# Performance work log

Hardware: AMD Instinct MI355X
Metric: run time of the kernel (lower is better)

Reference implementation:

```python
import jax, jax.numpy as jnp
import numpy as np

ALPHA_LO = float(np.exp(-1.0 / 5.0))   # 0.8187
ALPHA_HI = float(np.exp(-1.0 / 25.0))  # 0.9608
BN_EPS = 1e-5

B, T, D_IN, H = 32, 2000, 512, 512


def setup_inputs() -> dict:
    key = jax.random.key(0)
    ks = jax.random.split(key, 5)
    x = jax.random.normal(ks[0], (B, T, D_IN), dtype=jnp.float32)
    W = jax.random.normal(ks[1], (H, D_IN), dtype=jnp.float32) / np.sqrt(D_IN)
    b = jax.random.normal(ks[2], (H,), dtype=jnp.float32) * 0.01
    alpha = jax.random.uniform(ks[3], (H,), dtype=jnp.float32,
                               minval=ALPHA_LO, maxval=ALPHA_HI)
    gamma = jnp.ones((H,), dtype=jnp.float32)
    beta = jnp.zeros((H,), dtype=jnp.float32)
    ut0 = jax.random.uniform(ks[4], (B, H), dtype=jnp.float32)
    return {"x": x, "W": W, "b": b, "alpha": alpha,
            "gamma": gamma, "beta": beta, "ut0": ut0}


def reference(x, W, b, alpha, gamma, beta, ut0):
    # Linear: [B,T,Din] @ [Din,H] + b
    Wx = jnp.einsum("btd,hd->bth", x, W) + b
    # BatchNorm1d (training forward): stats over flattened (B*T) dim
    flat = Wx.reshape(-1, Wx.shape[-1])
    mean = flat.mean(axis=0)
    var = flat.var(axis=0)  # biased, as torch BN uses for normalization
    Wx = ((flat - mean) * jax.lax.rsqrt(var + BN_EPS) * gamma + beta).reshape(Wx.shape)
    # Readout cell: leaky integration + softmax accumulation over time
    a = jnp.clip(alpha, ALPHA_LO, ALPHA_HI)

    def step(carry, wxt):
        ut, acc = carry
        ut = a * ut + (1.0 - a) * wxt          # [B,H]
        acc = acc + jax.nn.softmax(ut, axis=1)
        return (ut, acc), None

    wx_t = jnp.transpose(Wx, (1, 0, 2))  # [T,B,H]
    (_, out), _ = jax.lax.scan(step, (ut0, jnp.zeros_like(ut0)), wx_t)
    return out[:, None, :]  # [B,1,H]
```

## Files before the change

### kernel.cpp

```cpp
#include <hip/hip_runtime.h>
#include <hip/hip_bf16.h>
#include <stdint.h>


namespace {
constexpr int kB = 32;
constexpr int kT = 2000;
constexpr int kD = 512;
constexpr int kH = 512;
constexpr int kM = kB * kT;
constexpr int kBM = 128;
constexpr int kNB = kM / kBM;
constexpr int kL = 20;
constexpr int kC = kT / kL;
constexpr float kALo = 0.81873075307798182f;
constexpr float kAHi = 0.96078943915232320f;

typedef __bf16 bf16x4 __attribute__((ext_vector_type(4)));
typedef __bf16 bf16x8 __attribute__((ext_vector_type(8)));
typedef float floatx16 __attribute__((ext_vector_type(16)));

__device__ __forceinline__ float bf2f(unsigned short u) {
  return __builtin_bit_cast(float, (unsigned)u << 16);
}
__device__ __forceinline__ float clipa(float a) {
  return fminf(fmaxf(a, kALo), kAHi);
}
__device__ __forceinline__ float pow20(float a) {
  const float a2 = a * a, a4 = a2 * a2, a5 = a4 * a;
  const float a10 = a5 * a5;
  return a10 * a10;
}
__device__ __forceinline__ void gld_lds16(const void* g, void* l) {
  __builtin_amdgcn_global_load_lds(
      (const __attribute__((address_space(1))) uint32_t*)g,
      (__attribute__((address_space(3))) uint32_t*)(uintptr_t)l, 16, 0, 0);
}

__global__ __launch_bounds__(256) void wcvt_k(const float* __restrict__ W,
                                              __bf16* __restrict__ Wbf) {
  const int t = blockIdx.x * 256 + threadIdx.x;
  const float4 a0 = ((const float4*)W)[t * 2];
  const float4 a1 = ((const float4*)W)[t * 2 + 1];
  bf16x8 v;
  v[0] = (__bf16)a0.x; v[1] = (__bf16)a0.y; v[2] = (__bf16)a0.z; v[3] = (__bf16)a0.w;
  v[4] = (__bf16)a1.x; v[5] = (__bf16)a1.y; v[6] = (__bf16)a1.z; v[7] = (__bf16)a1.w;
  const int h = t >> 6, k8 = t & 63;
  *(bf16x8*)(Wbf + ((size_t)k8 * 512 + h) * 8) = v;
}

__global__ __launch_bounds__(512, 2) void gemm_k(const float* __restrict__ X,
                                                 const __bf16* __restrict__ Wbf,
                                                 unsigned short* __restrict__ Wxb,
                                                 float* __restrict__ partial) {
  __shared__ alignas(16) __bf16 As2[2][4][128][8];
  __shared__ alignas(16) bf16x8 Bs2[2][2048];
  __shared__ float sred[2][kH];
  const int tid = threadIdx.x;
  const size_t row0 = (size_t)blockIdx.x * kBM;
  const int w = tid >> 6, L = tid & 63;
  const int ct0 = w * 2;
  const int lhalf = L >> 5, l32 = L & 31;
  const int arow = tid >> 2, akq = tid & 3;

  floatx16 acc[4][2] = {};
  const float* xptr = X + (row0 + arow) * kD + akq * 8;

  float4 a0 = *(const float4*)xptr;
  float4 a1 = *(const float4*)(xptr + 4);
#pragma unroll
  for (int j = 0; j < 4; ++j) {
    const int ci = j * 512 + tid;
    gld_lds16(Wbf + (size_t)ci * 8, (char*)&Bs2[0][0] + (size_t)ci * 16);
  }
  {
    bf16x8 av;
    av[0] = (__bf16)a0.x; av[1] = (__bf16)a0.y; av[2] = (__bf16)a0.z; av[3] = (__bf16)a0.w;
    av[4] = (__bf16)a1.x; av[5] = (__bf16)a1.y; av[6] = (__bf16)a1.z; av[7] = (__bf16)a1.w;
    *(bf16x8*)&As2[0][akq][arow][0] = av;
  }
  a0 = *(const float4*)(xptr + 32);
  a1 = *(const float4*)(xptr + 36);
  asm volatile("s_waitcnt vmcnt(2) lgkmcnt(0)" ::: "memory");
  __builtin_amdgcn_s_barrier();

#pragma unroll 1
  for (int s = 0; s < 16; ++s) {
    const int buf = s & 1;
    if (s < 15) {
#pragma unroll
      for (int j = 0; j < 4; ++j) {
        const int ci = j * 512 + tid;
        gld_lds16(Wbf + ((size_t)(s + 1) * 2048 + ci) * 8,
                  (char*)&Bs2[buf ^ 1][0] + (size_t)ci * 16);
      }
      bf16x8 av;
      av[0] = (__bf16)a0.x; av[1] = (__bf16)a0.y; av[2] = (__bf16)a0.z; av[3] = (__bf16)a0.w;
      av[4] = (__bf16)a1.x; av[5] = (__bf16)a1.y; av[6] = (__bf16)a1.z; av[7] = (__bf16)a1.w;
      *(bf16x8*)&As2[buf ^ 1][akq][arow][0] = av;
      if (s < 14) {
        a0 = *(const float4*)(xptr + (s + 2) * 32);
        a1 = *(const float4*)(xptr + (s + 2) * 32 + 4);
      }
    }
#pragma unroll
    for (int kh = 0; kh < 2; ++kh) {
      const int kq = kh * 2 + lhalf;
      const bf16x8 af0 = *(const bf16x8*)&As2[buf][kq][l32][0];
      const bf16x8 af1 = *(const bf16x8*)&As2[buf][kq][32 + l32][0];
      const bf16x8 af2 = *(const bf16x8*)&As2[buf][kq][64 + l32][0];
      const bf16x8 af3 = *(const bf16x8*)&As2[buf][kq][96 + l32][0];
      const bf16x8 b0 = Bs2[buf][kq * 512 + ct0 * 32 + l32];
      const bf16x8 b1 = Bs2[buf][kq * 512 + (ct0 + 1) * 32 + l32];
      acc[0][0] = __builtin_amdgcn_mfma_f32_32x32x16_bf16(af0, b0, acc[0][0], 0, 0, 0);
      acc[0][1] = __builtin_amdgcn_mfma_f32_32x32x16_bf16(af0, b1, acc[0][1], 0, 0, 0);
      acc[1][0] = __builtin_amdgcn_mfma_f32_32x32x16_bf16(af1, b0, acc[1][0], 0, 0, 0);
      acc[1][1] = __builtin_amdgcn_mfma_f32_32x32x16_bf16(af1, b1, acc[1][1], 0, 0, 0);
      acc[2][0] = __builtin_amdgcn_mfma_f32_32x32x16_bf16(af2, b0, acc[2][0], 0, 0, 0);
      acc[2][1] = __builtin_amdgcn_mfma_f32_32x32x16_bf16(af2, b1, acc[2][1], 0, 0, 0);
      acc[3][0] = __builtin_amdgcn_mfma_f32_32x32x16_bf16(af3, b0, acc[3][0], 0, 0, 0);
      acc[3][1] = __builtin_amdgcn_mfma_f32_32x32x16_bf16(af3, b1, acc[3][1], 0, 0, 0);
    }
    if (s < 15) {
      if (s < 14)
        asm volatile("s_waitcnt vmcnt(2) lgkmcnt(0)" ::: "memory");
      else
        asm volatile("s_waitcnt vmcnt(0) lgkmcnt(0)" ::: "memory");
      __builtin_amdgcn_s_barrier();
    }
  }

  __syncthreads();
  sred[0][tid] = 0.f;
  sred[1][tid] = 0.f;
  __syncthreads();
#pragma unroll
  for (int c = 0; c < 2; ++c) {
    float s = 0.f, q = 0.f;
#pragma unroll
    for (int rt = 0; rt < 4; ++rt) {
#pragma unroll
      for (int r = 0; r < 16; ++r) {
        const float v = acc[rt][c][r];
        s += v;
        q += v * v;
      }
    }
    s += __shfl_xor(s, 32);
    q += __shfl_xor(q, 32);
    if (lhalf == 0) {
      atomicAdd(&sred[0][(ct0 + c) * 32 + l32], s);
      atomicAdd(&sred[1][(ct0 + c) * 32 + l32], q);
    }
  }
#pragma unroll
  for (int rt = 0; rt < 4; ++rt) {
#pragma unroll
    for (int c = 0; c < 2; ++c) {
      const int col = (ct0 + c) * 32 + l32;
#pragma unroll
      for (int r = 0; r < 16; ++r) {
        const int row = rt * 32 + 4 * lhalf + (r & 3) + 8 * (r >> 2);
        const unsigned short u = __builtin_bit_cast(unsigned short, (__bf16)acc[rt][c][r]);
        const unsigned un = __shfl_down((unsigned)u, 1);
        if ((l32 & 1) == 0)
          *(unsigned*)(Wxb + (row0 + row) * (size_t)kH + col) = (unsigned)u | (un << 16);
      }
    }
  }
  __syncthreads();
  partial[(size_t)blockIdx.x * 1024 + tid] = sred[0][tid];
  partial[(size_t)blockIdx.x * 1024 + 512 + tid] = sred[1][tid];
}

__global__ __launch_bounds__(512) void red1_k(const float* __restrict__ partial,
                                              float* __restrict__ sums) {
  const int tid = threadIdx.x;
  const int r0 = blockIdx.x * 20;
  float s0 = 0.f, s1 = 0.f;
#pragma unroll 5
  for (int r = 0; r < 20; ++r) {
    s0 += partial[(size_t)(r0 + r) * 1024 + tid];
    s1 += partial[(size_t)(r0 + r) * 1024 + 512 + tid];
  }
  atomicAdd(&sums[tid], s0);
  atomicAdd(&sums[kH + tid], s1);
}

__global__ __launch_bounds__(512) void finalize_k(const float* __restrict__ sums,
                                                  const float* __restrict__ alpha,
                                                  const float* __restrict__ gamma,
                                                  const float* __restrict__ beta,
                                                  float* __restrict__ prm) {
  const int h = threadIdx.x;
  const float inv_n = 1.0f / (float)kM;
  const float mean = sums[h] * inv_n;
  const float var = sums[kH + h] * inv_n - mean * mean;
  const float sc = gamma[h] * rsqrtf(var + 1e-5f);
  const float sh = beta[h] - mean * sc;
  const float a = clipa(alpha[h]);
  prm[h] = sc;
  prm[kH + h] = sh;
  prm[2 * kH + h] = a;
  prm[3 * kH + h] = 1.0f - a;
  prm[4 * kH + h] = pow20(a);
}

__global__ __launch_bounds__(512) void agg_raw_k(const unsigned short* __restrict__ Wxb,
                                                 const float* __restrict__ alpha,
                                                 float* __restrict__ vbuf) {
  const int bc = blockIdx.x;
  const int b = bc / kC, c = bc % kC;
  const int h = threadIdx.x;
  const float a = clipa(alpha[h]);
  const float oma = 1.0f - a;
  const unsigned short* base = Wxb + ((size_t)b * kT + (size_t)c * kL) * kH + h;
  float v = 0.f;
#pragma unroll
  for (int i = 0; i < kL; ++i)
    v = a * v + oma * bf2f(base[(size_t)i * kH]);
  vbuf[(size_t)bc * kH + h] = v;
}

__global__ __launch_bounds__(512) void scan_k(const float* __restrict__ ut0,
                                              const float* __restrict__ alpha,
                                              const float* __restrict__ prm,
                                              float* __restrict__ vbuf) {
  const int b = blockIdx.x;
  const int h = threadIdx.x;
  const float a20 = pow20(clipa(alpha[h]));
  const float sc = prm[h];
  const float shc = prm[kH + h] * (1.0f - a20);
  float u = ut0[(size_t)b * kH + h];
  float vc[10];
#pragma unroll 1
  for (int cb = 0; cb < kC; cb += 10) {
#pragma unroll
    for (int j = 0; j < 10; ++j)
      vc[j] = vbuf[((size_t)b * kC + cb + j) * kH + h];
#pragma unroll
    for (int j = 0; j < 10; ++j) {
      vbuf[((size_t)b * kC + cb + j) * kH + h] = u;
      u = a20 * u + sc * vc[j] + shc;
    }
  }
}

__global__ __launch_bounds__(512) void soft_k(const unsigned short* __restrict__ Wxb,
                                              const float* __restrict__ prm,
                                              const float* __restrict__ ustart,
                                              float* __restrict__ accp) {
  __shared__ float part[kL][9];
  __shared__ float zinv[kL];
  const int bc = blockIdx.x;
  const int b = bc / kC, c = bc % kC;
  const int h = threadIdx.x;
  const int wv = h >> 6, lane = h & 63;
  const float sc = prm[h], sh = prm[kH + h];
  const float a = prm[2 * kH + h], oma = prm[3 * kH + h];
  float u = ustart[(size_t)bc * kH + h];
  const unsigned short* base = Wxb + ((size_t)b * kT + (size_t)c * kL) * kH + h;
  float e[kL];
#pragma unroll
  for (int i = 0; i < kL; ++i) {
    const float wvx = bf2f(base[(size_t)i * kH]) * sc + sh;
    u = a * u + oma * wvx;
    e[i] = __expf(u);
  }
#pragma unroll
  for (int i = 0; i < kL; ++i) {
    float s = e[i];
#pragma unroll
    for (int off = 32; off > 0; off >>= 1) s += __shfl_xor(s, off);
    if (lane == 0) part[i][wv] = s;
  }
  __syncthreads();
  if (h < kL) {
    float s = 0.f;
#pragma unroll
    for (int j = 0; j < 8; ++j) s += part[h][j];
    zinv[h] = 1.0f / s;
  }
  __syncthreads();
  float acc = 0.f;
#pragma unroll
  for (int i = 0; i < kL; ++i) acc += e[i] * zinv[i];
  accp[(size_t)bc * kH + h] = acc;
}

__global__ __launch_bounds__(512) void out_red_k(const float* __restrict__ accp,
                                                 float* __restrict__ out) {
  const int b = blockIdx.x;
  const int h = threadIdx.x;
  float s = 0.f;
#pragma unroll 4
  for (int c = 0; c < kC; ++c) s += accp[((size_t)b * kC + c) * kH + h];
  out[(size_t)b * kH + h] = s;
}

}

extern "C" void kernel_launch(void* const* d_in, const int* in_sizes, int n_in,
                              void* d_out, int out_size, void* d_ws, size_t ws_size,
                              hipStream_t stream) {
  const float* x = (const float*)d_in[0];
  const float* Wm = (const float*)d_in[1];
  const float* alpha = (const float*)d_in[3];
  const float* gamma = (const float*)d_in[4];
  const float* beta = (const float*)d_in[5];
  const float* ut0 = (const float*)d_in[6];
  float* out = (float*)d_out;

  float* wsp = (float*)d_ws;
  float* vbuf = wsp;
  float* accp = vbuf + (size_t)kB * kC * kH;
  float* partial = accp + (size_t)kB * kC * kH;
  float* sums = partial + (size_t)1000 * 1024;
  float* prm = sums + 2 * kH;
  __bf16* Wbf = (__bf16*)(prm + 5 * kH);
  unsigned short* Wxb = (unsigned short*)(Wbf + (size_t)kH * kD);

  hipMemsetAsync(sums, 0, 2 * kH * sizeof(float), stream);
  wcvt_k<<<128, 256, 0, stream>>>(Wm, Wbf);
  gemm_k<<<kNB, 512, 0, stream>>>(x, Wbf, Wxb, partial);
  agg_raw_k<<<kB * kC, 512, 0, stream>>>(Wxb, alpha, vbuf);
  red1_k<<<25, 512, 0, stream>>>(partial, sums);
  finalize_k<<<1, 512, 0, stream>>>(sums, alpha, gamma, beta, prm);
  scan_k<<<kB, 512, 0, stream>>>(ut0, alpha, prm, vbuf);
  soft_k<<<kB * kC, 512, 0, stream>>>(Wxb, prm, vbuf, accp);
  out_red_k<<<kB, 512, 0, stream>>>(accp, out);
}
```

Before: 301.1 us.

## Fuse chunk aggregation into GEMM epilogue and merge scan, softmax, and output reduction

Chunk length drops to 16 so each chunk lines up with the MFMA accumulator row layout. The GEMM epilogue now computes the decay-weighted per-chunk sums directly from the accumulators, which removes the separate aggregation kernel that re-read the bf16 activations. Finalize and scan are merged into one kernel. The softmax kernel handles groups of five chunks and adds its result atomically into the output, which removes the final reduction kernel. The cost is a heavier GEMM epilogue with extra shuffles and global stores, plus atomics on the output that require a memset of the output first.

```diff
diff --git a/kernel.cpp b/kernel.cpp
--- a/kernel.cpp
+++ b/kernel.cpp
@@ -11,12 +11,13 @@
 constexpr int kM = kB * kT;
 constexpr int kBM = 128;
 constexpr int kNB = kM / kBM;
-constexpr int kL = 20;
+constexpr int kL = 16;
 constexpr int kC = kT / kL;
+constexpr int kG = 5;
+constexpr int kNG = kC / kG;
 constexpr float kALo = 0.81873075307798182f;
 constexpr float kAHi = 0.96078943915232320f;
 
-typedef __bf16 bf16x4 __attribute__((ext_vector_type(4)));
 typedef __bf16 bf16x8 __attribute__((ext_vector_type(8)));
 typedef float floatx16 __attribute__((ext_vector_type(16)));
 
@@ -26,10 +27,9 @@
 __device__ __forceinline__ float clipa(float a) {
   return fminf(fmaxf(a, kALo), kAHi);
 }
-__device__ __forceinline__ float pow20(float a) {
-  const float a2 = a * a, a4 = a2 * a2, a5 = a4 * a;
-  const float a10 = a5 * a5;
-  return a10 * a10;
+__device__ __forceinline__ float pow16(float a) {
+  const float a2 = a * a, a4 = a2 * a2, a8 = a4 * a4;
+  return a8 * a8;
 }
 __device__ __forceinline__ void gld_lds16(const void* g, void* l) {
   __builtin_amdgcn_global_load_lds(
@@ -51,7 +51,9 @@
 
 __global__ __launch_bounds__(512, 2) void gemm_k(const float* __restrict__ X,
                                                  const __bf16* __restrict__ Wbf,
+                                                 const float* __restrict__ alpha,
                                                  unsigned short* __restrict__ Wxb,
+                                                 float* __restrict__ vbuf,
                                                  float* __restrict__ partial) {
   __shared__ alignas(16) __bf16 As2[2][4][128][8];
   __shared__ alignas(16) bf16x8 Bs2[2][2048];
@@ -153,6 +155,35 @@
       atomicAdd(&sred[1][(ct0 + c) * 32 + l32], q);
     }
   }
+
+#pragma unroll
+  for (int c = 0; c < 2; ++c) {
+    const int col = (ct0 + c) * 32 + l32;
+    const float a = clipa(alpha[col]);
+    const float oma = 1.0f - a;
+    const float a2 = a * a, a4 = a2 * a2, a8 = a4 * a4;
+    float wgt[8];
+    wgt[0] = a8 * a2 * a; wgt[1] = a8 * a2; wgt[2] = a8 * a; wgt[3] = a8;
+    wgt[4] = a2 * a;      wgt[5] = a2;      wgt[6] = a;      wgt[7] = 1.0f;
+    const float mult = (lhalf == 0) ? a4 * oma : oma;
+#pragma unroll
+    for (int j = 0; j < 8; ++j) wgt[j] *= mult;
+#pragma unroll
+    for (int rt = 0; rt < 4; ++rt) {
+#pragma unroll
+      for (int c32 = 0; c32 < 2; ++c32) {
+        float S = 0.f;
+#pragma unroll
+        for (int j = 0; j < 8; ++j) S += wgt[j] * acc[rt][c][c32 * 8 + j];
+        S += __shfl_xor(S, 32);
+        if (lhalf == 0) {
+          const int g = (int)(row0 >> 4) + rt * 2 + c32;
+          vbuf[(size_t)g * kH + col] = S;
+        }
+      }
+    }
+  }
+
 #pragma unroll
   for (int rt = 0; rt < 4; ++rt) {
 #pragma unroll
@@ -187,115 +218,88 @@
   atomicAdd(&sums[kH + tid], s1);
 }
 
-__global__ __launch_bounds__(512) void finalize_k(const float* __restrict__ sums,
+__global__ __launch_bounds__(512) void fin_scan_k(const float* __restrict__ sums,
                                                   const float* __restrict__ alpha,
                                                   const float* __restrict__ gamma,
                                                   const float* __restrict__ beta,
-                                                  float* __restrict__ prm) {
+                                                  const float* __restrict__ ut0,
+                                                  float* __restrict__ prm,
+                                                  const float* __restrict__ vbuf,
+                                                  float* __restrict__ ustart) {
   const int h = threadIdx.x;
+  const int b = blockIdx.x;
   const float inv_n = 1.0f / (float)kM;
   const float mean = sums[h] * inv_n;
   const float var = sums[kH + h] * inv_n - mean * mean;
   const float sc = gamma[h] * rsqrtf(var + 1e-5f);
   const float sh = beta[h] - mean * sc;
   const float a = clipa(alpha[h]);
-  prm[h] = sc;
-  prm[kH + h] = sh;
-  prm[2 * kH + h] = a;
-  prm[3 * kH + h] = 1.0f - a;
-  prm[4 * kH + h] = pow20(a);
-}
-
-__global__ __launch_bounds__(512) void agg_raw_k(const unsigned short* __restrict__ Wxb,
-                                                 const float* __restrict__ alpha,
-                                                 float* __restrict__ vbuf) {
-  const int bc = blockIdx.x;
-  const int b = bc / kC, c = bc % kC;
-  const int h = threadIdx.x;
-  const float a = clipa(alpha[h]);
-  const float oma = 1.0f - a;
-  const unsigned short* base = Wxb + ((size_t)b * kT + (size_t)c * kL) * kH + h;
-  float v = 0.f;
-#pragma unroll
-  for (int i = 0; i < kL; ++i)
-    v = a * v + oma * bf2f(base[(size_t)i * kH]);
-  vbuf[(size_t)bc * kH + h] = v;
-}
-
-__global__ __launch_bounds__(512) void scan_k(const float* __restrict__ ut0,
-                                              const float* __restrict__ alpha,
-                                              const float* __restrict__ prm,
-                                              float* __restrict__ vbuf) {
-  const int b = blockIdx.x;
-  const int h = threadIdx.x;
-  const float a20 = pow20(clipa(alpha[h]));
-  const float sc = prm[h];
-  const float shc = prm[kH + h] * (1.0f - a20);
+  if (b == 0) {
+    prm[h] = sc;
+    prm[kH + h] = sh;
+    prm[2 * kH + h] = a;
+    prm[3 * kH + h] = 1.0f - a;
+  }
+  const float a16 = pow16(a);
+  const float shc = sh * (1.0f - a16);
   float u = ut0[(size_t)b * kH + h];
-  float vc[10];
+  float vc[kG];
 #pragma unroll 1
-  for (int cb = 0; cb < kC; cb += 10) {
-#pragma unroll
-    for (int j = 0; j < 10; ++j)
+  for (int cb = 0; cb < kC; cb += kG) {
+#pragma unroll
+    for (int j = 0; j < kG; ++j)
       vc[j] = vbuf[((size_t)b * kC + cb + j) * kH + h];
-#pragma unroll
-    for (int j = 0; j < 10; ++j) {
-      vbuf[((size_t)b * kC + cb + j) * kH + h] = u;
-      u = a20 * u + sc * vc[j] + shc;
-    }
+    ustart[((size_t)b * kNG + cb / kG) * kH + h] = u;
+#pragma unroll
+    for (int j = 0; j < kG; ++j) u = a16 * u + sc * vc[j] + shc;
   }
 }
 
 __global__ __launch_bounds__(512) void soft_k(const unsigned short* __restrict__ Wxb,
                                               const float* __restrict__ prm,
                                               const float* __restrict__ ustart,
-                                              float* __restrict__ accp) {
+                                              float* __restrict__ out) {
   __shared__ float part[kL][9];
   __shared__ float zinv[kL];
   const int bc = blockIdx.x;
-  const int b = bc / kC, c = bc % kC;
+  const int b = bc / kNG, grp = bc % kNG;
   const int h = threadIdx.x;
   const int wv = h >> 6, lane = h & 63;
   const float sc = prm[h], sh = prm[kH + h];
   const float a = prm[2 * kH + h], oma = prm[3 * kH + h];
   float u = ustart[(size_t)bc * kH + h];
-  const unsigned short* base = Wxb + ((size_t)b * kT + (size_t)c * kL) * kH + h;
-  float e[kL];
-#pragma unroll
-  for (int i = 0; i < kL; ++i) {
-    const float wvx = bf2f(base[(size_t)i * kH]) * sc + sh;
-    u = a * u + oma * wvx;
-    e[i] = __expf(u);
-  }
-#pragma unroll
-  for (int i = 0; i < kL; ++i) {
-    float s = e[i];
-#pragma unroll
-    for (int off = 32; off > 0; off >>= 1) s += __shfl_xor(s, off);
-    if (lane == 0) part[i][wv] = s;
-  }
-  __syncthreads();
-  if (h < kL) {
-    float s = 0.f;
-#pragma unroll
-    for (int j = 0; j < 8; ++j) s += part[h][j];
-    zinv[h] = 1.0f / s;
-  }
-  __syncthreads();
+  const unsigned short* base =
+      Wxb + ((size_t)b * kT + (size_t)grp * kG * kL) * kH + h;
   float acc = 0.f;
-#pragma unroll
-  for (int i = 0; i < kL; ++i) acc += e[i] * zinv[i];
-  accp[(size_t)bc * kH + h] = acc;
-}
-
-__global__ __launch_bounds__(512) void out_red_k(const float* __restrict__ accp,
-                                                 float* __restrict__ out) {
-  const int b = blockIdx.x;
-  const int h = threadIdx.x;
-  float s = 0.f;
-#pragma unroll 4
-  for (int c = 0; c < kC; ++c) s += accp[((size_t)b * kC + c) * kH + h];
-  out[(size_t)b * kH + h] = s;
+#pragma unroll 1
+  for (int cc = 0; cc < kG; ++cc) {
+    float e[kL];
+#pragma unroll
+    for (int i = 0; i < kL; ++i) {
+      const float wvx = bf2f(base[(size_t)(cc * kL + i) * kH]) * sc + sh;
+      u = a * u + oma * wvx;
+      e[i] = __expf(u);
+    }
+#pragma unroll
+    for (int i = 0; i < kL; ++i) {
+      float s = e[i];
+#pragma unroll
+      for (int off = 32; off > 0; off >>= 1) s += __shfl_xor(s, off);
+      if (lane == 0) part[i][wv] = s;
+    }
+    __syncthreads();
+    if (h < kL) {
+      float s = 0.f;
+#pragma unroll
+      for (int j = 0; j < 8; ++j) s += part[h][j];
+      zinv[h] = 1.0f / s;
+    }
+    __syncthreads();
+#pragma unroll
+    for (int i = 0; i < kL; ++i) acc += e[i] * zinv[i];
+    __syncthreads();
+  }
+  atomicAdd(&out[(size_t)b * kH + h], acc);
 }
 
 }
@@ -313,20 +317,18 @@
 
   float* wsp = (float*)d_ws;
   float* vbuf = wsp;
-  float* accp = vbuf + (size_t)kB * kC * kH;
-  float* partial = accp + (size_t)kB * kC * kH;
-  float* sums = partial + (size_t)1000 * 1024;
+  float* ustart = vbuf + (size_t)kB * kC * kH;
+  float* partial = ustart + (size_t)kB * kNG * kH;
+  float* sums = partial + (size_t)500 * 1024;
   float* prm = sums + 2 * kH;
-  __bf16* Wbf = (__bf16*)(prm + 5 * kH);
+  __bf16* Wbf = (__bf16*)(prm + 4 * kH);
   unsigned short* Wxb = (unsigned short*)(Wbf + (size_t)kH * kD);
 
   hipMemsetAsync(sums, 0, 2 * kH * sizeof(float), stream);
+  hipMemsetAsync(out, 0, (size_t)kB * kH * sizeof(float), stream);
   wcvt_k<<<128, 256, 0, stream>>>(Wm, Wbf);
-  gemm_k<<<kNB, 512, 0, stream>>>(x, Wbf, Wxb, partial);
-  agg_raw_k<<<kB * kC, 512, 0, stream>>>(Wxb, alpha, vbuf);
+  gemm_k<<<kNB, 512, 0, stream>>>(x, Wbf, alpha, Wxb, vbuf, partial);
   red1_k<<<25, 512, 0, stream>>>(partial, sums);
-  finalize_k<<<1, 512, 0, stream>>>(sums, alpha, gamma, beta, prm);
-  scan_k<<<kB, 512, 0, stream>>>(ut0, alpha, prm, vbuf);
-  soft_k<<<kB * kC, 512, 0, stream>>>(Wxb, prm, vbuf, accp);
-  out_red_k<<<kB, 512, 0, stream>>>(accp, out);
-}
+  fin_scan_k<<<kB, 512, 0, stream>>>(sums, alpha, gamma, beta, ut0, prm, vbuf, ustart);
+  soft_k<<<kB * kNG, 512, 0, stream>>>(Wxb, prm, ustart, out);
+}
```

Measured after the change: 301.4 us. About the same (+0.1%).
